# Kernel tuning notes

Measured on AMD Instinct MI355X. Metric: run time of the kernel, lower is better.

The kernel has to match this reference:

```python
import jax, jax.numpy as jnp
import numpy as np

EPS = 1e-12
SAMPLE_SIZES = (100, 50)  # hardcoded in the torch module


def setup_inputs() -> dict:
    key = jax.random.key(0)
    k1, k2, k3, k4 = jax.random.split(key, 4)
    N, E, C_IN, C_HID, C_OUT = 50000, 1600000, 256, 64, 128
    x = jax.random.normal(k1, (N, C_IN), dtype=jnp.float32)
    edge_index = jax.random.randint(k2, (2, E), 0, N, dtype=jnp.int64)
    W1 = jax.random.normal(k3, (C_IN, C_HID), dtype=jnp.float32) / np.sqrt(C_IN)
    b1 = jnp.zeros((C_HID,), dtype=jnp.float32)
    W2 = jax.random.normal(k4, (C_HID, C_OUT), dtype=jnp.float32) / np.sqrt(C_HID)
    b2 = jnp.zeros((C_OUT,), dtype=jnp.float32)
    return {"x": x, "edge_index": edge_index, "W1": W1, "b1": b1, "W2": W2, "b2": b2}


def _sample_mask(edge_index, num_samples, key):
    """Keep at most num_samples random out-edges per source node (fixed-shape mask)."""
    src = edge_index[0]
    E = src.shape[0]
    pri = jax.random.uniform(key, (E,))
    order = jnp.lexsort((pri, src))            # group by src, random order within group
    src_sorted = src[order]
    first = jnp.searchsorted(src_sorted, src_sorted, side="left")
    rank = jnp.arange(E) - first               # rank within each src group
    keep_sorted = rank < num_samples
    mask = jnp.zeros((E,), dtype=jnp.float32).at[order].set(keep_sorted.astype(jnp.float32))
    return mask


def _gcn_conv(x, edge_index, edge_weight, W, b, num_nodes):
    """PyG GCNConv: self-loops + symmetric deg^-1/2 normalization, aggregate at dst."""
    h = x @ W                                   # [N, out]
    src, dst = edge_index[0], edge_index[1]
    loop = jnp.arange(num_nodes, dtype=src.dtype)
    src_f = jnp.concatenate([src, loop])
    dst_f = jnp.concatenate([dst, loop])
    w_f = jnp.concatenate([edge_weight, jnp.ones((num_nodes,), dtype=edge_weight.dtype)])
    deg = jax.ops.segment_sum(w_f, dst_f, num_segments=num_nodes)
    dinv = jnp.where(deg > 0, jax.lax.rsqrt(jnp.maximum(deg, EPS)), 0.0)
    norm = w_f * dinv[src_f] * dinv[dst_f]      # [E+N]
    msgs = h[src_f] * norm[:, None]             # gather + scale (memory bound)
    out = jax.ops.segment_sum(msgs, dst_f, num_segments=num_nodes)
    return out + b


def reference(x, edge_index, W1, b1, W2, b2):
    num_nodes = x.shape[0]
    skey = jax.random.key(42)
    sk1, sk2 = jax.random.split(skey)
    m1 = _sample_mask(edge_index, SAMPLE_SIZES[0], sk1)
    m2 = _sample_mask(edge_index, SAMPLE_SIZES[1], sk2)
    h = _gcn_conv(x, edge_index, m1, W1, b1, num_nodes)
    h = jax.nn.relu(h)
    h = h / jnp.maximum(jnp.linalg.norm(h, axis=-1, keepdims=True), EPS)  # F.normalize(p=2)
    out = _gcn_conv(h, edge_index, m2, W2, b2, num_nodes)
    return out
```

## Files before the change

### kernel.cpp

```cpp
#include <hip/hip_runtime.h>

typedef unsigned int u32;
typedef unsigned short u16;
typedef unsigned long long u64;
typedef __attribute__((ext_vector_type(8))) short bh8;
typedef __attribute__((ext_vector_type(4))) float f4;

#define HMAX 1024
#define MAXD 128
#define SB_CAP 24576
#define DB_CAP 6144
#define SBCHUNK 8192
#define SPLIT 8
#define G1S 72
#define DROP_CAP 32768
#define CPAD 16

__device__ inline f4 mfma16(bh8 a, bh8 b, f4 c) {
  return __builtin_amdgcn_mfma_f32_16x16x32_bf16(a, b, c, 0, 0, 0);
}

__host__ __device__ inline void tf2x32(u32 k0, u32 k1, u32 x0, u32 x1, u32& o0, u32& o1) {
  u32 ks2 = k0 ^ k1 ^ 0x1BD11BDAu;
#define ROTL32(x,d) (((x)<<(d))|((x)>>(32-(d))))
#define TFR(r) { x0 += x1; x1 = ROTL32(x1,(r)); x1 ^= x0; }
  x0 += k0; x1 += k1;
  TFR(13) TFR(15) TFR(26) TFR(6)
  x0 += k1; x1 += ks2 + 1u;
  TFR(17) TFR(29) TFR(16) TFR(24)
  x0 += ks2; x1 += k0 + 2u;
  TFR(13) TFR(15) TFR(26) TFR(6)
  x0 += k0; x1 += k1 + 3u;
  TFR(17) TFR(29) TFR(16) TFR(24)
  x0 += k1; x1 += ks2 + 4u;
  TFR(13) TFR(15) TFR(26) TFR(6)
  x0 += ks2; x1 += k0 + 5u;
  o0 = x0; o1 = x1;
#undef TFR
#undef ROTL32
}

__device__ inline u16 f2bf(float f) {
  u32 u = __float_as_uint(f);
  return (u16)((u + 0x7FFFu + ((u >> 16) & 1u)) >> 16);
}
__device__ inline float bflo(u32 u) { return __uint_as_float(u << 16); }
__device__ inline float bfhi(u32 u) { return __uint_as_float(u & 0xFFFF0000u); }

#define ACC8(uv, wt) \
  a0 = fmaf(wt, bflo(uv.x), a0); a1 = fmaf(wt, bfhi(uv.x), a1); \
  a2 = fmaf(wt, bflo(uv.y), a2); a3 = fmaf(wt, bfhi(uv.y), a3); \
  a4 = fmaf(wt, bflo(uv.z), a4); a5 = fmaf(wt, bfhi(uv.z), a5); \
  a6 = fmaf(wt, bflo(uv.w), a6); a7 = fmaf(wt, bfhi(uv.w), a7);

struct BinS { u32 lsrc[128]; u32 lbase[128]; u32 ldst[512]; u32 dbase[512]; };
struct GemS { u16 xs[64 * G1S]; u16 ws[64 * G1S]; };

__global__ __launch_bounds__(256) void k_mega1(const int* __restrict__ ei, int E,
                                               const float* __restrict__ x, int N,
                                               const float* __restrict__ W1, const float* __restrict__ W2,
                                               int* __restrict__ srcCnt, u32* __restrict__ srcRec,
                                               int* __restrict__ dstCnt, u64* __restrict__ dstRec,
                                               u16* __restrict__ h1b, u16* __restrict__ W2t, int nBin) {
  __shared__ __align__(16) char smem[sizeof(GemS)];
  int t = threadIdx.x;
  int bid = blockIdx.x;
  int nGemm = (N + 63) >> 6;

  if (bid < nBin) {
    BinS& S = *(BinS*)smem;
    if (t < 128) S.lsrc[t] = 0;
    for (int v = t; v < 512; v += 256) S.ldst[v] = 0;
    __syncthreads();
    int lo = bid * SBCHUNK;
    int hi = min(lo + SBCHUNK, E);
    bool fast = ((E & 3) == 0);

    auto loadE = [&](int e0, int nv, int* sv, int* dv) {
      if (nv == 8 && fast) {
        int4 a0 = *((const int4*)(ei + e0));
        int4 a1 = *((const int4*)(ei + e0 + 4));
        int4 b0 = *((const int4*)(ei + E + e0));
        int4 b1 = *((const int4*)(ei + E + e0 + 4));
        sv[0]=a0.x; sv[1]=a0.y; sv[2]=a0.z; sv[3]=a0.w; sv[4]=a1.x; sv[5]=a1.y; sv[6]=a1.z; sv[7]=a1.w;
        dv[0]=b0.x; dv[1]=b0.y; dv[2]=b0.z; dv[3]=b0.w; dv[4]=b1.x; dv[5]=b1.y; dv[6]=b1.z; dv[7]=b1.w;
      } else {
        for (int j = 0; j < nv; ++j) { sv[j] = ei[e0 + j]; dv[j] = ei[E + e0 + j]; }
      }
    };

    for (int sub = 0; sub < SBCHUNK; sub += 2048) {
      int e0 = lo + sub + 8 * t;
      int nv = min(8, hi - e0); if (nv < 0) nv = 0;
      int sv[8], dv[8];
      loadE(e0, nv, sv, dv);
      for (int j = 0; j < nv; ++j) {
        atomicAdd(&S.lsrc[sv[j] >> 9], 1u);
        atomicAdd(&S.ldst[dv[j] >> 7], 1u);
      }
    }
    __syncthreads();
    if (t < 128) {
      u32 c = S.lsrc[t];
      if (c) S.lbase[t] = (u32)atomicAdd(&srcCnt[t * CPAD], (int)c);
      S.lsrc[t] = 0;
    }
    for (int v = t; v < 512; v += 256) {
      u32 cd = S.ldst[v];
      if (cd) S.dbase[v] = (u32)atomicAdd(&dstCnt[v * CPAD], (int)cd);
      S.ldst[v] = 0;
    }
    __syncthreads();
    for (int sub = 0; sub < SBCHUNK; sub += 2048) {
      int e0 = lo + sub + 8 * t;
      int nv = min(8, hi - e0); if (nv < 0) nv = 0;
      int sv[8], dv[8];
      loadE(e0, nv, sv, dv);
      for (int j = 0; j < nv; ++j) {
        int s = sv[j], d = dv[j];
        u32 i = (u32)(e0 + j);
        int bs = s >> 9;
        u32 slot = S.lbase[bs] + atomicAdd(&S.lsrc[bs], 1u);
        if (slot < SB_CAP) srcRec[(size_t)bs * SB_CAP + slot] = ((u32)(s & 511) << 21) | i;
        int bd = d >> 7;
        u32 slot2 = S.dbase[bd] + atomicAdd(&S.ldst[bd], 1u);
        if (slot2 < DB_CAP)
          dstRec[(size_t)bd * DB_CAP + slot2] = ((u64)(d & 127) << 37) | ((u64)(u32)s << 21) | i;
      }
    }
  } else if (bid < nBin + nGemm) {
    GemS& G = *(GemS*)smem;
    int wv = t >> 6, lane = t & 63;
    int qd = lane >> 4, md = lane & 15;
    int m0 = (bid - nBin) * 64;
    if (m0 >= N) return;
    f4 acc[4] = {};
    for (int ks = 0; ks < 256; ks += 64) {
      __syncthreads();
#pragma unroll
      for (int i = 0; i < 4; ++i) {
        int f = t + 256 * i;
        int r = f >> 4, c4 = f & 15;
        int grow = m0 + r; if (grow >= N) grow = N - 1;
        float4 v = ((const float4*)x)[(size_t)grow * 64 + (ks >> 2) + c4];
        u32 p0 = (u32)f2bf(v.x) | ((u32)f2bf(v.y) << 16);
        u32 p1 = (u32)f2bf(v.z) | ((u32)f2bf(v.w) << 16);
        *((uint2*)(G.xs + r * G1S + c4 * 4)) = make_uint2(p0, p1);
      }
#pragma unroll
      for (int i = 0; i < 4; ++i) {
        int f = t + 256 * i;
        int k = f >> 4, c4 = f & 15;
        float4 v = ((const float4*)W1)[(ks + k) * 16 + c4];
        int n0 = c4 * 4;
        G.ws[(n0 + 0) * G1S + k] = f2bf(v.x);
        G.ws[(n0 + 1) * G1S + k] = f2bf(v.y);
        G.ws[(n0 + 2) * G1S + k] = f2bf(v.z);
        G.ws[(n0 + 3) * G1S + k] = f2bf(v.w);
      }
      __syncthreads();
#pragma unroll
      for (int kk = 0; kk < 64; kk += 32) {
        bh8 af = *((const bh8*)(G.xs + (16 * wv + md) * G1S + kk + qd * 8));
#pragma unroll
        for (int nt = 0; nt < 4; ++nt) {
          bh8 bf = *((const bh8*)(G.ws + (nt * 16 + md) * G1S + kk + qd * 8));
          acc[nt] = mfma16(af, bf, acc[nt]);
        }
      }
    }
#pragma unroll
    for (int nt = 0; nt < 4; ++nt)
#pragma unroll
      for (int r = 0; r < 4; ++r) {
        int row = m0 + 16 * wv + qd * 4 + r;
        if (row < N) h1b[(size_t)row * 64 + nt * 16 + md] = f2bf(acc[nt][r]);
      }
  } else {
    for (int e = t; e < 64 * 128; e += 256) {
      int n = e & 127, k = e >> 7;
      W2t[n * 64 + k] = f2bf(W2[k * 128 + n]);
    }
  }
}

__global__ __launch_bounds__(256) void k_shist(const int* __restrict__ srcCnt, const u32* __restrict__ srcRec,
                                               int* __restrict__ outdegB) {
  int bk = blockIdx.x >> 3;
  int part = blockIdx.x & (SPLIT - 1);
  int total = min(srcCnt[bk * CPAD], SB_CAP);
  int lo = total * part / SPLIT;
  int hi = total * (part + 1) / SPLIT;
  __shared__ u32 cnt[512];
  int t = threadIdx.x;
  cnt[t] = 0; cnt[t + 256] = 0;
  __syncthreads();
  const u32* R = srcRec + (size_t)bk * SB_CAP;
  for (int i = lo + t; i < hi; i += 256) atomicAdd(&cnt[R[i] >> 21], 1u);
  __syncthreads();
  int base = bk * 512;
  for (int v = t; v < 512; v += 256) {
    u32 c = cnt[v];
    if (c) atomicAdd(&outdegB[base + v], (int)c);
  }
}

__global__ __launch_bounds__(256) void k_hdetect(const int* __restrict__ outdegB, u32* __restrict__ idAB,
                                                 int* __restrict__ hcA, int* __restrict__ hcB,
                                                 const int* __restrict__ dstCnt, int* __restrict__ bucketBase,
                                                 int* __restrict__ dptr, int nbD, int N) {
  int t = threadIdx.x;
  if (blockIdx.x == 0) {
    __shared__ int sc[512], tp[512];
    for (int i = t; i < 512; i += 256) sc[i] = (i < nbD) ? min(dstCnt[i * CPAD], DB_CAP) : 0;
    __syncthreads();
    for (int off = 1; off < 512; off <<= 1) {
      for (int i = t; i < 512; i += 256) tp[i] = sc[i] + ((i >= off) ? sc[i - off] : 0);
      __syncthreads();
      for (int i = t; i < 512; i += 256) sc[i] = tp[i];
      __syncthreads();
    }
    for (int i = t; i < 512; i += 256) {
      if (i < nbD) bucketBase[i] = (i == 0) ? 0 : sc[i - 1];
    }
    if (t == 0) {
      int tot = sc[nbD - 1];
      bucketBase[nbD] = tot;
      dptr[N] = tot;
    }
  }
  int v = blockIdx.x * 256 + t;
  if (v >= N) return;
  int dg = outdegB[v];
  u32 pk = 0;
  if (dg > 50) {
    int idb = atomicAdd(hcB, 1);
    if (idb < HMAX) pk = (u32)(idb + 1);
    if (dg > 100) {
      int ida = atomicAdd(hcA, 1);
      if (ida < HMAX) pk |= (u32)(ida + 1) << 16;
    }
  }
  idAB[v] = pk;
}

__global__ __launch_bounds__(256) void k_hfill(const int* __restrict__ srcCnt, const u32* __restrict__ srcRec,
                                               const u32* __restrict__ idAB,
                                               int* __restrict__ bcA, u64* __restrict__ bukA,
                                               int* __restrict__ bcB, u64* __restrict__ bukB,
                                               u32 kaA, u32 kbA, u32 kaB, u32 kbB) {
  int bk = blockIdx.x >> 3;
  int part = blockIdx.x & (SPLIT - 1);
  int total = min(srcCnt[bk * CPAD], SB_CAP);
  int lo = total * part / SPLIT;
  int hi = total * (part + 1) / SPLIT;
  const u32* R = srcRec + (size_t)bk * SB_CAP;
  int base = bk * 512;
  for (int i = lo + threadIdx.x; i < hi; i += 256) {
    u32 r = R[i];
    u32 pk = idAB[base + (int)(r >> 21)];
    if (pk) {
      u32 e = r & 0x1FFFFFu;
      int idb = (int)(pk & 0xFFFFu) - 1;
      if (idb >= 0) {
        u32 w0, w1; tf2x32(kaB, kbB, 0u, e, w0, w1);
        int slot = atomicAdd(&bcB[idb], 1);
        if (slot < MAXD) bukB[(size_t)idb * MAXD + slot] = ((u64)((w0 ^ w1) >> 9) << 32) | e;
      }
      int ida = (int)(pk >> 16) - 1;
      if (ida >= 0) {
        u32 w0, w1; tf2x32(kaA, kbA, 0u, e, w0, w1);
        int slot = atomicAdd(&bcA[ida], 1);
        if (slot < MAXD) bukA[(size_t)ida * MAXD + slot] = ((u64)((w0 ^ w1) >> 9) << 32) | e;
      }
    }
  }
}

__global__ __launch_bounds__(256) void k_rank2(const int* __restrict__ hcA, const int* __restrict__ bcA,
                                               const u64* __restrict__ bukA,
                                               const int* __restrict__ hcB, const int* __restrict__ bcB,
                                               const u64* __restrict__ bukB,
                                               int* __restrict__ dropCnt, u32* __restrict__ dropList) {
  bool isA = blockIdx.x < (HMAX / 4);
  int bx = isA ? blockIdx.x : blockIdx.x - HMAX / 4;
  const int* hcount = isA ? hcA : hcB;
  const int* bcount = isA ? bcA : bcB;
  const u64* bucket = isA ? bukA : bukB;
  int S = isA ? 100 : 50;
  u32 bit = isA ? 1u : 2u;
  int wid = (bx * 256 + (int)threadIdx.x) >> 6;
  int lane = threadIdx.x & 63;
  int hc = hcount[0]; if (hc > HMAX) hc = HMAX;
  if (wid >= hc) return;
  int d = bcount[wid]; if (d > MAXD) d = MAXD;
  const u64* B = bucket + (size_t)wid * MAXD;
  for (int i = lane; i < d; i += 64) {
    u64 ki = B[i];
    int rank = 0;
    for (int j = 0; j < d; ++j) rank += (B[j] < ki) ? 1 : 0;
    if (rank >= S) {
      int idx = atomicAdd(dropCnt, 1);
      if (idx < DROP_CAP) dropList[idx] = ((u32)ki & 0x1FFFFFu) | (bit << 21);
    }
  }
}

__global__ __launch_bounds__(256) void k_phase2(const int* __restrict__ bucketBase,
                                                const int* __restrict__ dstCnt,
                                                const u64* __restrict__ dstRec,
                                                const int* __restrict__ dropCnt,
                                                const u32* __restrict__ dropList,
                                                u32* __restrict__ entries, int* __restrict__ dptr,
                                                float* __restrict__ dinv1, float* __restrict__ dinv2, int N) {
  int b = blockIdx.x;
  int base = bucketBase[b];
  int cnt0 = min(dstCnt[b * CPAD], DB_CAP);
  const u64* R = dstRec + (size_t)b * DB_CAP;
  __shared__ u32 cnt[128];
  __shared__ u32 htab[4096];
  __shared__ u32 ws2[2];
  __shared__ u32 earr[DB_CAP];
  int t = threadIdx.x;
  if (t < 128) cnt[t] = 0;
  for (int i = t; i < 4096; i += 256) htab[i] = 0xFFFFFFFFu;
  __syncthreads();
  int dc = min(dropCnt[0], 3072);
  for (int i = t; i < dc; i += 256) {
    u32 pk = dropList[i];
    u32 key = pk & 0x1FFFFFu;
    u32 h = (key * 2654435761u) >> 20;
    while (true) {
      u32 old = atomicCAS(&htab[h], 0xFFFFFFFFu, pk);
      if (old == 0xFFFFFFFFu) break;
      if ((old & 0x1FFFFFu) == key) { atomicOr(&htab[h], pk & 0x00600000u); break; }
      h = (h + 1) & 4095;
    }
  }
  __syncthreads();
  for (int i = t; i < cnt0; i += 256) {
    u64 r = R[i];
    u32 dl = (u32)(r >> 37) & 127u;
    u32 key = (u32)r & 0x1FFFFFu;
    u32 drop = 0;
    u32 h = (key * 2654435761u) >> 20;
    while (true) {
      u32 v = htab[h];
      if (v == 0xFFFFFFFFu) break;
      if ((v & 0x1FFFFFu) == key) { drop = (v >> 21) & 3u; break; }
      h = (h + 1) & 4095;
    }
    u32 src = (u32)(r >> 21) & 0xFFFFu;
    earr[i] = src | (drop << 16) | (dl << 18);
    u32 add = 1u + ((1u - (drop & 1u)) << 10) + ((1u - ((drop >> 1) & 1u)) << 20);
    atomicAdd(&cnt[dl], add);
  }
  __syncthreads();
  u32 c0 = (t < 128) ? cnt[t] : 0;
  u32 tot = c0 & 1023u;
  int lane = t & 63, w = t >> 6;
  u32 incl = tot;
  for (int off = 1; off < 64; off <<= 1) {
    u32 nbv = (u32)__shfl_up((int)incl, off, 64);
    if (lane >= off) incl += nbv;
  }
  if (lane == 63 && w == 0) ws2[0] = incl;
  __syncthreads();
  u32 excl = incl - tot + ((w == 1) ? ws2[0] : 0u);
  int v0 = b * 128 + t;
  if (t < 128 && v0 < N) {
    dptr[v0] = base + (int)excl;
    dinv1[v0] = 1.0f / sqrtf((float)(((c0 >> 10) & 1023u) + 1u));
    dinv2[v0] = 1.0f / sqrtf((float)(((c0 >> 20) & 1023u) + 1u));
  }
  __syncthreads();
  if (t < 128) cnt[t] = excl;
  __syncthreads();
  for (int i = t; i < cnt0; i += 256) {
    u32 p = earr[i];
    u32 dl = (p >> 18) & 127u;
    u32 drop = (p >> 16) & 3u;
    u32 src = p & 0xFFFFu;
    u32 slot = atomicAdd(&cnt[dl], 1u);
    entries[base + slot] = src | ((drop & 1u) ? 0u : (1u << 30)) | ((drop & 2u) ? 0u : (1u << 31));
  }
}

__global__ __launch_bounds__(256) void k_conv1n(const int* __restrict__ ptr, const u32* __restrict__ entries,
                                                const float* __restrict__ dinv1, const uint4* __restrict__ h1q,
                                                const float* __restrict__ b1, uint4* __restrict__ hnbq, int N) {
  int wid = (blockIdx.x * 256 + threadIdx.x) >> 6;
  if (wid >= N) return;
  int lane = threadIdx.x & 63;
  int lo8 = lane & 7, grp = lane >> 3;
  int beg = ptr[wid], end = ptr[wid + 1];
  float a0 = 0.f, a1 = 0.f, a2 = 0.f, a3 = 0.f, a4 = 0.f, a5 = 0.f, a6 = 0.f, a7 = 0.f;
  for (int cb = beg; cb < end; cb += 64) {
    int idx = cb + lane;
    float wgt = 0.f; int s = 0;
    if (idx < end) {
      u32 e = entries[idx];
      s = (int)(e & 0xFFFFu);
      if (e & (1u << 30)) wgt = dinv1[s];
    }
    int nq = (min(64, end - cb) + 7) >> 3;
    float wA = __shfl(wgt, grp, 64); int sA = __shfl(s, grp, 64);
    uint4 uA = h1q[(size_t)sA * 8 + lo8];
    float wB = 0.f; uint4 uB = uA;
    if (nq > 1) {
      wB = __shfl(wgt, grp + 8, 64); int sB = __shfl(s, grp + 8, 64);
      uB = h1q[(size_t)sB * 8 + lo8];
    }
    for (int i = 2; i < nq; ++i) {
      int jc = grp + 8 * i;
      float wC = __shfl(wgt, jc, 64); int sC = __shfl(s, jc, 64);
      uint4 uC = h1q[(size_t)sC * 8 + lo8];
      ACC8(uA, wA)
      wA = wB; uA = uB; wB = wC; uB = uC;
    }
    ACC8(uA, wA)
    if (nq > 1) { ACC8(uB, wB) }
  }
#pragma unroll
  for (int off = 8; off < 64; off <<= 1) {
    a0 += __shfl_xor(a0, off, 64); a1 += __shfl_xor(a1, off, 64);
    a2 += __shfl_xor(a2, off, 64); a3 += __shfl_xor(a3, off, 64);
    a4 += __shfl_xor(a4, off, 64); a5 += __shfl_xor(a5, off, 64);
    a6 += __shfl_xor(a6, off, 64); a7 += __shfl_xor(a7, off, 64);
  }
  float dv = dinv1[wid];
  uint4 uo = h1q[(size_t)wid * 8 + lo8];
  a0 = fmaf(dv, bflo(uo.x), a0); a1 = fmaf(dv, bfhi(uo.x), a1);
  a2 = fmaf(dv, bflo(uo.y), a2); a3 = fmaf(dv, bfhi(uo.y), a3);
  a4 = fmaf(dv, bflo(uo.z), a4); a5 = fmaf(dv, bfhi(uo.z), a5);
  a6 = fmaf(dv, bflo(uo.w), a6); a7 = fmaf(dv, bfhi(uo.w), a7);
  float4 bbA = ((const float4*)b1)[lo8 * 2];
  float4 bbB = ((const float4*)b1)[lo8 * 2 + 1];
  float o0 = fmaxf(fmaf(dv, a0, bbA.x), 0.f);
  float o1 = fmaxf(fmaf(dv, a1, bbA.y), 0.f);
  float o2 = fmaxf(fmaf(dv, a2, bbA.z), 0.f);
  float o3 = fmaxf(fmaf(dv, a3, bbA.w), 0.f);
  float o4 = fmaxf(fmaf(dv, a4, bbB.x), 0.f);
  float o5 = fmaxf(fmaf(dv, a5, bbB.y), 0.f);
  float o6 = fmaxf(fmaf(dv, a6, bbB.z), 0.f);
  float o7 = fmaxf(fmaf(dv, a7, bbB.w), 0.f);
  float ss = fmaf(o0, o0, fmaf(o1, o1, fmaf(o2, o2, o3 * o3)))
           + fmaf(o4, o4, fmaf(o5, o5, fmaf(o6, o6, o7 * o7)));
#pragma unroll
  for (int off = 1; off < 8; off <<= 1) ss += __shfl_xor(ss, off, 8);
  float sc = 1.f / fmaxf(sqrtf(ss), 1e-12f);
  if (lane < 8) {
    uint4 pv;
    pv.x = (u32)f2bf(o0 * sc) | ((u32)f2bf(o1 * sc) << 16);
    pv.y = (u32)f2bf(o2 * sc) | ((u32)f2bf(o3 * sc) << 16);
    pv.z = (u32)f2bf(o4 * sc) | ((u32)f2bf(o5 * sc) << 16);
    pv.w = (u32)f2bf(o6 * sc) | ((u32)f2bf(o7 * sc) << 16);
    hnbq[(size_t)wid * 8 + lo8] = pv;
  }
}

__global__ __launch_bounds__(256) void k_agg2(const int* __restrict__ ptr, const u32* __restrict__ entries,
                                              const float* __restrict__ dinv2, const uint4* __restrict__ hnq,
                                              uint4* __restrict__ agg2q, int N) {
  int wid = (blockIdx.x * 256 + threadIdx.x) >> 6;
  if (wid >= N) return;
  int lane = threadIdx.x & 63;
  int lo8 = lane & 7, grp = lane >> 3;
  int beg = ptr[wid], end = ptr[wid + 1];
  float a0 = 0.f, a1 = 0.f, a2 = 0.f, a3 = 0.f, a4 = 0.f, a5 = 0.f, a6 = 0.f, a7 = 0.f;
  for (int cb = beg; cb < end; cb += 64) {
    int idx = cb + lane;
    float wgt = 0.f; int s = 0;
    if (idx < end) {
      u32 e = entries[idx];
      s = (int)(e & 0xFFFFu);
      if (e & (1u << 31)) wgt = dinv2[s];
    }
    int nq = (min(64, end - cb) + 7) >> 3;
    float wA = __shfl(wgt, grp, 64); int sA = __shfl(s, grp, 64);
    uint4 uA = hnq[(size_t)sA * 8 + lo8];
    float wB = 0.f; uint4 uB = uA;
    if (nq > 1) {
      wB = __shfl(wgt, grp + 8, 64); int sB = __shfl(s, grp + 8, 64);
      uB = hnq[(size_t)sB * 8 + lo8];
    }
    for (int i = 2; i < nq; ++i) {
      int jc = grp + 8 * i;
      float wC = __shfl(wgt, jc, 64); int sC = __shfl(s, jc, 64);
      uint4 uC = hnq[(size_t)sC * 8 + lo8];
      ACC8(uA, wA)
      wA = wB; uA = uB; wB = wC; uB = uC;
    }
    ACC8(uA, wA)
    if (nq > 1) { ACC8(uB, wB) }
  }
#pragma unroll
  for (int off = 8; off < 64; off <<= 1) {
    a0 += __shfl_xor(a0, off, 64); a1 += __shfl_xor(a1, off, 64);
    a2 += __shfl_xor(a2, off, 64); a3 += __shfl_xor(a3, off, 64);
    a4 += __shfl_xor(a4, off, 64); a5 += __shfl_xor(a5, off, 64);
    a6 += __shfl_xor(a6, off, 64); a7 += __shfl_xor(a7, off, 64);
  }
  float dv = dinv2[wid];
  uint4 uo = hnq[(size_t)wid * 8 + lo8];
  a0 = fmaf(dv, bflo(uo.x), a0); a1 = fmaf(dv, bfhi(uo.x), a1);
  a2 = fmaf(dv, bflo(uo.y), a2); a3 = fmaf(dv, bfhi(uo.y), a3);
  a4 = fmaf(dv, bflo(uo.z), a4); a5 = fmaf(dv, bfhi(uo.z), a5);
  a6 = fmaf(dv, bflo(uo.w), a6); a7 = fmaf(dv, bfhi(uo.w), a7);
  if (lane < 8) {
    uint4 pv;
    pv.x = (u32)f2bf(dv * a0) | ((u32)f2bf(dv * a1) << 16);
    pv.y = (u32)f2bf(dv * a2) | ((u32)f2bf(dv * a3) << 16);
    pv.z = (u32)f2bf(dv * a4) | ((u32)f2bf(dv * a5) << 16);
    pv.w = (u32)f2bf(dv * a6) | ((u32)f2bf(dv * a7) << 16);
    agg2q[(size_t)wid * 8 + lo8] = pv;
  }
}

#define G2S 72
__global__ __launch_bounds__(256) void k_gemm2f(const u16* __restrict__ aggb, const u16* __restrict__ W2t,
                                                const float* __restrict__ b2, float* __restrict__ out, int N) {
  __shared__ u16 hs[64 * G2S];
  __shared__ u16 ws[128 * G2S];
  int t = threadIdx.x;
  int wv = t >> 6, lane = t & 63;
  int qd = lane >> 4, md = lane & 15;
  int m0 = blockIdx.x * 64;
#pragma unroll
  for (int i = 0; i < 2; ++i) {
    int cc = t + 256 * i;
    int r = cc >> 3, kc = (cc & 7) * 8;
    int grow = m0 + r; if (grow >= N) grow = N - 1;
    *((uint4*)(hs + r * G2S + kc)) = *((const uint4*)(aggb + (size_t)grow * 64 + kc));
  }
#pragma unroll
  for (int i = 0; i < 4; ++i) {
    int cc = t + 256 * i;
    int n = cc >> 3, kc = (cc & 7) * 8;
    *((uint4*)(ws + n * G2S + kc)) = *((const uint4*)(W2t + n * 64 + kc));
  }
  __syncthreads();
  f4 acc[8] = {};
#pragma unroll
  for (int kk = 0; kk < 64; kk += 32) {
    bh8 af = *((const bh8*)(hs + (16 * wv + md) * G2S + kk + qd * 8));
#pragma unroll
    for (int nt = 0; nt < 8; ++nt) {
      bh8 bf = *((const bh8*)(ws + (nt * 16 + md) * G2S + kk + qd * 8));
      acc[nt] = mfma16(af, bf, acc[nt]);
    }
  }
#pragma unroll
  for (int nt = 0; nt < 8; ++nt) {
    float bv = b2[nt * 16 + md];
#pragma unroll
    for (int r = 0; r < 4; ++r) {
      int row = m0 + 16 * wv + qd * 4 + r;
      if (row < N) out[(size_t)row * 128 + nt * 16 + md] = acc[nt][r] + bv;
    }
  }
}

extern "C" void kernel_launch(void* const* d_in, const int* in_sizes, int n_in,
                              void* d_out, int out_size, void* d_ws, size_t ws_size,
                              hipStream_t stream) {
  const float* x  = (const float*)d_in[0];
  const int*   ei = (const int*)d_in[1];
  const float* W1 = (const float*)d_in[2];
  const float* b1 = (const float*)d_in[3];
  const float* W2 = (const float*)d_in[4];
  const float* b2 = (const float*)d_in[5];
  const int N = in_sizes[0] / 256;
  const int E = in_sizes[1] / 2;
  const int nbS = (N + 511) >> 9;
  const int nbD = (N + 127) >> 7;

  u32 sk1a, sk1b, sk2a, sk2b;
  tf2x32(0u, 42u, 0u, 0u, sk1a, sk1b);
  tf2x32(0u, 42u, 0u, 1u, sk2a, sk2b);

  char* p = (char*)d_ws;
  auto alloc = [&](size_t bytes) { char* r = p; p += (bytes + 255) & ~(size_t)255; return r; };
  int* dstCnt      = (int*)alloc((size_t)512 * CPAD * 4);
  int* srcCnt      = (int*)alloc((size_t)128 * CPAD * 4);
  int* hcbA        = (int*)alloc((size_t)(1 + HMAX) * 4);
  int* hcbB        = (int*)alloc((size_t)(1 + HMAX) * 4);
  int* outdegB     = (int*)alloc((size_t)nbS * 512 * 4);
  int* dropCnt     = (int*)alloc(256);
  char* zero_end = p;
  u32* dropList = (u32*)alloc((size_t)DROP_CAP * 4);
  u32* idAB     = (u32*)alloc((size_t)nbS * 512 * 4);
  u16* h1b      = (u16*)alloc((size_t)N * 64 * 2);
  u16* hnb      = (u16*)alloc((size_t)N * 64 * 2);
  u16* agg2b    = (u16*)alloc((size_t)N * 64 * 2);
  float* dinv1  = (float*)alloc((size_t)N * 4);
  float* dinv2  = (float*)alloc((size_t)N * 4);
  int* dptr     = (int*)alloc((size_t)(N + 1) * 4);
  int* bucketBase = (int*)alloc(513 * 4);
  u32* entries  = (u32*)alloc((size_t)E * 4);
  u32* srcRec   = (u32*)alloc((size_t)nbS * SB_CAP * 4);
  u64* dstRec   = (u64*)alloc((size_t)nbD * DB_CAP * 8);
  u64* bukA     = (u64*)alloc((size_t)HMAX * MAXD * 8);
  u64* bukB     = (u64*)alloc((size_t)HMAX * MAXD * 8);
  u16* W2t      = (u16*)alloc(64 * 128 * 2);

  int* hcA = hcbA; int* bcA = hcbA + 1;
  int* hcB = hcbB; int* bcB = hcbB + 1;

  hipMemsetAsync(dstCnt, 0x00, (size_t)(zero_end - (char*)dstCnt), stream);

  const int nBin = (E + SBCHUNK - 1) / SBCHUNK;
  const int nGemm = (N + 63) / 64;
  k_mega1<<<nBin + nGemm + 1, 256, 0, stream>>>(ei, E, x, N, W1, W2,
                                                srcCnt, srcRec, dstCnt, dstRec, h1b, W2t, nBin);
  k_shist<<<nbS * SPLIT, 256, 0, stream>>>(srcCnt, srcRec, outdegB);
  k_hdetect<<<(N + 255) / 256, 256, 0, stream>>>(outdegB, idAB, hcA, hcB, dstCnt, bucketBase,
                                                 dptr, nbD, N);
  k_hfill<<<nbS * SPLIT, 256, 0, stream>>>(srcCnt, srcRec, idAB, bcA, bukA, bcB, bukB,
                                           sk1a, sk1b, sk2a, sk2b);
  k_rank2<<<HMAX / 2, 256, 0, stream>>>(hcA, bcA, bukA, hcB, bcB, bukB, dropCnt, dropList);
  k_phase2<<<nbD, 256, 0, stream>>>(bucketBase, dstCnt, dstRec, dropCnt, dropList,
                                    entries, dptr, dinv1, dinv2, N);
  k_conv1n<<<(N * 64 + 255) / 256, 256, 0, stream>>>(dptr, entries, dinv1, (const uint4*)h1b, b1,
                                                     (uint4*)hnb, N);
  k_agg2<<<(N * 64 + 255) / 256, 256, 0, stream>>>(dptr, entries, dinv2, (const uint4*)hnb,
                                                   (uint4*)agg2b, N);
  k_gemm2f<<<(N + 63) / 64, 256, 0, stream>>>(agg2b, W2t, b2, (float*)d_out, N);
}
```

Baseline: 260.9 us.

## Fuse middle preprocessing kernels into one cooperative kernel with grid syncs

Replaces five back-to-back launches (source histogram, hub detection, hub bucket fill, rank/drop, destination phase2) with a single cooperative kernel on a fixed 768-workgroup grid. Phases are separated by grid.sync, and the old launches remain as a fallback if the cooperative launch fails. The aim is to remove per-launch overhead and tail gaps between the small kernels. The cost is grid-sync barriers, a large shared-memory union that may limit occupancy, and grid-stride loops over fewer workgroups. SBCHUNK is also halved, which doubles the binning blocks in the first kernel.

```diff
diff --git a/kernel.cpp b/kernel.cpp
--- a/kernel.cpp
+++ b/kernel.cpp
@@ -1,4 +1,6 @@
 #include <hip/hip_runtime.h>
+#include <hip/hip_cooperative_groups.h>
+namespace cg = cooperative_groups;
 
 typedef unsigned int u32;
 typedef unsigned short u16;
@@ -10,11 +12,12 @@
 #define MAXD 128
 #define SB_CAP 24576
 #define DB_CAP 6144
-#define SBCHUNK 8192
+#define SBCHUNK 4096
 #define SPLIT 8
 #define G1S 72
 #define DROP_CAP 32768
 #define CPAD 16
+#define GRID_MID 768
 
 __device__ inline f4 mfma16(bh8 a, bh8 b, f4 c) {
   return __builtin_amdgcn_mfma_f32_16x16x32_bf16(a, b, c, 0, 0, 0);
@@ -181,6 +184,209 @@
       int n = e & 127, k = e >> 7;
       W2t[n * 64 + k] = f2bf(W2[k * 128 + n]);
     }
+  }
+}
+
+__global__ __launch_bounds__(256) void k_mid(const int* __restrict__ srcCnt, const u32* __restrict__ srcRec,
+                                             int* __restrict__ outdegB, u32* __restrict__ idAB,
+                                             int* __restrict__ hcA, int* __restrict__ hcB,
+                                             const int* __restrict__ dstCnt, int* __restrict__ bucketBase,
+                                             int* __restrict__ dptr,
+                                             int* __restrict__ bcA, u64* __restrict__ bukA,
+                                             int* __restrict__ bcB, u64* __restrict__ bukB,
+                                             u32 kaA, u32 kbA, u32 kaB, u32 kbB,
+                                             int* __restrict__ dropCnt, u32* __restrict__ dropList,
+                                             const u64* __restrict__ dstRec,
+                                             u32* __restrict__ entries,
+                                             float* __restrict__ dinv1, float* __restrict__ dinv2,
+                                             int nbS, int nbD, int N) {
+  cg::grid_group grid = cg::this_grid();
+  __shared__ union {
+    u32 hist[512];
+    struct { int sc[512]; int tp[512]; } scan;
+    struct { u32 cnt[128]; u32 ws2[2]; u32 htab[4096]; u32 earr[DB_CAP]; } p2;
+  } MS;
+  int t = threadIdx.x;
+  int nWG = (int)gridDim.x;
+
+  for (int c = blockIdx.x; c < nbS * SPLIT; c += nWG) {
+    int bk = c >> 3, part = c & (SPLIT - 1);
+    int total = min(srcCnt[bk * CPAD], SB_CAP);
+    int lo = total * part / SPLIT;
+    int hi = total * (part + 1) / SPLIT;
+    MS.hist[t] = 0; MS.hist[t + 256] = 0;
+    __syncthreads();
+    const u32* R = srcRec + (size_t)bk * SB_CAP;
+    for (int i = lo + t; i < hi; i += 256) atomicAdd(&MS.hist[R[i] >> 21], 1u);
+    __syncthreads();
+    int base = bk * 512;
+    for (int v = t; v < 512; v += 256) {
+      u32 cc = MS.hist[v];
+      if (cc) atomicAdd(&outdegB[base + v], (int)cc);
+    }
+    __syncthreads();
+  }
+  grid.sync();
+
+  if (blockIdx.x == 0) {
+    for (int i = t; i < 512; i += 256) MS.scan.sc[i] = (i < nbD) ? min(dstCnt[i * CPAD], DB_CAP) : 0;
+    __syncthreads();
+    for (int off = 1; off < 512; off <<= 1) {
+      for (int i = t; i < 512; i += 256) MS.scan.tp[i] = MS.scan.sc[i] + ((i >= off) ? MS.scan.sc[i - off] : 0);
+      __syncthreads();
+      for (int i = t; i < 512; i += 256) MS.scan.sc[i] = MS.scan.tp[i];
+      __syncthreads();
+    }
+    for (int i = t; i < 512; i += 256) {
+      if (i < nbD) bucketBase[i] = (i == 0) ? 0 : MS.scan.sc[i - 1];
+    }
+    if (t == 0) {
+      int tot = MS.scan.sc[nbD - 1];
+      bucketBase[nbD] = tot;
+      dptr[N] = tot;
+    }
+  }
+  for (int vb = blockIdx.x * 256; vb < N; vb += nWG * 256) {
+    int v = vb + t;
+    if (v < N) {
+      int dg = outdegB[v];
+      u32 pk = 0;
+      if (dg > 50) {
+        int idb = atomicAdd(hcB, 1);
+        if (idb < HMAX) pk = (u32)(idb + 1);
+        if (dg > 100) {
+          int ida = atomicAdd(hcA, 1);
+          if (ida < HMAX) pk |= (u32)(ida + 1) << 16;
+        }
+      }
+      idAB[v] = pk;
+    }
+  }
+  grid.sync();
+
+  for (int c = blockIdx.x; c < nbS * SPLIT; c += nWG) {
+    int bk = c >> 3, part = c & (SPLIT - 1);
+    int total = min(srcCnt[bk * CPAD], SB_CAP);
+    int lo = total * part / SPLIT;
+    int hi = total * (part + 1) / SPLIT;
+    const u32* R = srcRec + (size_t)bk * SB_CAP;
+    int base = bk * 512;
+    for (int i = lo + t; i < hi; i += 256) {
+      u32 r = R[i];
+      u32 pk = idAB[base + (int)(r >> 21)];
+      if (pk) {
+        u32 e = r & 0x1FFFFFu;
+        int idb = (int)(pk & 0xFFFFu) - 1;
+        if (idb >= 0) {
+          u32 w0, w1; tf2x32(kaB, kbB, 0u, e, w0, w1);
+          int slot = atomicAdd(&bcB[idb], 1);
+          if (slot < MAXD) bukB[(size_t)idb * MAXD + slot] = ((u64)((w0 ^ w1) >> 9) << 32) | e;
+        }
+        int ida = (int)(pk >> 16) - 1;
+        if (ida >= 0) {
+          u32 w0, w1; tf2x32(kaA, kbA, 0u, e, w0, w1);
+          int slot = atomicAdd(&bcA[ida], 1);
+          if (slot < MAXD) bukA[(size_t)ida * MAXD + slot] = ((u64)((w0 ^ w1) >> 9) << 32) | e;
+        }
+      }
+    }
+  }
+  grid.sync();
+
+  for (int c = blockIdx.x; c < HMAX / 2; c += nWG) {
+    bool isA = c < (HMAX / 4);
+    int bx = isA ? c : c - HMAX / 4;
+    const int* hcount = isA ? hcA : hcB;
+    const int* bcount = isA ? bcA : bcB;
+    const u64* bucket = isA ? bukA : bukB;
+    int Sq = isA ? 100 : 50;
+    u32 bit = isA ? 1u : 2u;
+    int wid = (bx * 256 + t) >> 6;
+    int lane = t & 63;
+    int hc = hcount[0]; if (hc > HMAX) hc = HMAX;
+    if (wid < hc) {
+      int d = bcount[wid]; if (d > MAXD) d = MAXD;
+      const u64* B = bucket + (size_t)wid * MAXD;
+      for (int i = lane; i < d; i += 64) {
+        u64 ki = B[i];
+        int rank = 0;
+        for (int j = 0; j < d; ++j) rank += (B[j] < ki) ? 1 : 0;
+        if (rank >= Sq) {
+          int idx = atomicAdd(dropCnt, 1);
+          if (idx < DROP_CAP) dropList[idx] = ((u32)ki & 0x1FFFFFu) | (bit << 21);
+        }
+      }
+    }
+  }
+  grid.sync();
+
+  for (int b = blockIdx.x; b < nbD; b += nWG) {
+    int base = bucketBase[b];
+    int cnt0 = min(dstCnt[b * CPAD], DB_CAP);
+    const u64* R = dstRec + (size_t)b * DB_CAP;
+    if (t < 128) MS.p2.cnt[t] = 0;
+    for (int i = t; i < 4096; i += 256) MS.p2.htab[i] = 0xFFFFFFFFu;
+    __syncthreads();
+    int dc = min(dropCnt[0], 3072);
+    for (int i = t; i < dc; i += 256) {
+      u32 pk = dropList[i];
+      u32 key = pk & 0x1FFFFFu;
+      u32 h = (key * 2654435761u) >> 20;
+      while (true) {
+        u32 old = atomicCAS(&MS.p2.htab[h], 0xFFFFFFFFu, pk);
+        if (old == 0xFFFFFFFFu) break;
+        if ((old & 0x1FFFFFu) == key) { atomicOr(&MS.p2.htab[h], pk & 0x00600000u); break; }
+        h = (h + 1) & 4095;
+      }
+    }
+    __syncthreads();
+    for (int i = t; i < cnt0; i += 256) {
+      u64 r = R[i];
+      u32 dl = (u32)(r >> 37) & 127u;
+      u32 key = (u32)r & 0x1FFFFFu;
+      u32 drop = 0;
+      u32 h = (key * 2654435761u) >> 20;
+      while (true) {
+        u32 v = MS.p2.htab[h];
+        if (v == 0xFFFFFFFFu) break;
+        if ((v & 0x1FFFFFu) == key) { drop = (v >> 21) & 3u; break; }
+        h = (h + 1) & 4095;
+      }
+      u32 src = (u32)(r >> 21) & 0xFFFFu;
+      MS.p2.earr[i] = src | (drop << 16) | (dl << 18);
+      u32 add = 1u + ((1u - (drop & 1u)) << 10) + ((1u - ((drop >> 1) & 1u)) << 20);
+      atomicAdd(&MS.p2.cnt[dl], add);
+    }
+    __syncthreads();
+    u32 c0 = (t < 128) ? MS.p2.cnt[t] : 0;
+    u32 tot = c0 & 1023u;
+    int lane = t & 63, w = t >> 6;
+    u32 incl = tot;
+    for (int off = 1; off < 64; off <<= 1) {
+      u32 nbv = (u32)__shfl_up((int)incl, off, 64);
+      if (lane >= off) incl += nbv;
+    }
+    if (lane == 63 && w == 0) MS.p2.ws2[0] = incl;
+    __syncthreads();
+    u32 excl = incl - tot + ((w == 1) ? MS.p2.ws2[0] : 0u);
+    int vn = b * 128 + t;
+    if (t < 128 && vn < N) {
+      dptr[vn] = base + (int)excl;
+      dinv1[vn] = 1.0f / sqrtf((float)(((c0 >> 10) & 1023u) + 1u));
+      dinv2[vn] = 1.0f / sqrtf((float)(((c0 >> 20) & 1023u) + 1u));
+    }
+    __syncthreads();
+    if (t < 128) MS.p2.cnt[t] = excl;
+    __syncthreads();
+    for (int i = t; i < cnt0; i += 256) {
+      u32 p = MS.p2.earr[i];
+      u32 dl = (p >> 18) & 127u;
+      u32 drop = (p >> 16) & 3u;
+      u32 src = p & 0xFFFFu;
+      u32 slot = atomicAdd(&MS.p2.cnt[dl], 1u);
+      entries[base + slot] = src | ((drop & 1u) ? 0u : (1u << 30)) | ((drop & 2u) ? 0u : (1u << 31));
+    }
+    __syncthreads();
   }
 }
 
@@ -613,14 +819,27 @@
   const int nGemm = (N + 63) / 64;
   k_mega1<<<nBin + nGemm + 1, 256, 0, stream>>>(ei, E, x, N, W1, W2,
                                                 srcCnt, srcRec, dstCnt, dstRec, h1b, W2t, nBin);
-  k_shist<<<nbS * SPLIT, 256, 0, stream>>>(srcCnt, srcRec, outdegB);
-  k_hdetect<<<(N + 255) / 256, 256, 0, stream>>>(outdegB, idAB, hcA, hcB, dstCnt, bucketBase,
-                                                 dptr, nbD, N);
-  k_hfill<<<nbS * SPLIT, 256, 0, stream>>>(srcCnt, srcRec, idAB, bcA, bukA, bcB, bukB,
-                                           sk1a, sk1b, sk2a, sk2b);
-  k_rank2<<<HMAX / 2, 256, 0, stream>>>(hcA, bcA, bukA, hcB, bcB, bukB, dropCnt, dropList);
-  k_phase2<<<nbD, 256, 0, stream>>>(bucketBase, dstCnt, dstRec, dropCnt, dropList,
-                                    entries, dptr, dinv1, dinv2, N);
+
+  int nbS_v = nbS, nbD_v = nbD, N_v = N;
+  void* margs[] = { (void*)&srcCnt, (void*)&srcRec, (void*)&outdegB, (void*)&idAB,
+                    (void*)&hcA, (void*)&hcB, (void*)&dstCnt, (void*)&bucketBase, (void*)&dptr,
+                    (void*)&bcA, (void*)&bukA, (void*)&bcB, (void*)&bukB,
+                    (void*)&sk1a, (void*)&sk1b, (void*)&sk2a, (void*)&sk2b,
+                    (void*)&dropCnt, (void*)&dropList, (void*)&dstRec, (void*)&entries,
+                    (void*)&dinv1, (void*)&dinv2, (void*)&nbS_v, (void*)&nbD_v, (void*)&N_v };
+  hipError_t cerr = hipLaunchCooperativeKernel((void*)k_mid, dim3(GRID_MID), dim3(256),
+                                               margs, 0, stream);
+  if (cerr != hipSuccess) {
+    k_shist<<<nbS * SPLIT, 256, 0, stream>>>(srcCnt, srcRec, outdegB);
+    k_hdetect<<<(N + 255) / 256, 256, 0, stream>>>(outdegB, idAB, hcA, hcB, dstCnt, bucketBase,
+                                                   dptr, nbD, N);
+    k_hfill<<<nbS * SPLIT, 256, 0, stream>>>(srcCnt, srcRec, idAB, bcA, bukA, bcB, bukB,
+                                             sk1a, sk1b, sk2a, sk2b);
+    k_rank2<<<HMAX / 2, 256, 0, stream>>>(hcA, bcA, bukA, hcB, bcB, bukB, dropCnt, dropList);
+    k_phase2<<<nbD, 256, 0, stream>>>(bucketBase, dstCnt, dstRec, dropCnt, dropList,
+                                      entries, dptr, dinv1, dinv2, N);
+  }
+
   k_conv1n<<<(N * 64 + 255) / 256, 256, 0, stream>>>(dptr, entries, dinv1, (const uint4*)h1b, b1,
                                                      (uint4*)hnb, N);
   k_agg2<<<(N * 64 + 255) / 256, 256, 0, stream>>>(dptr, entries, dinv2, (const uint4*)hnb,
```

Result: slower. 586.2 us (+124.7%).
